# Performance work log

Hardware: AMD Instinct MI355X
Metric: run time of the kernel (lower is better)

## Reference

```python
import jax, jax.numpy as jnp
import numpy as np

V = 20000
D = 128
N_PAIRS = 65536
LOG_EPS = 1e-8


def setup_inputs() -> dict:
    key = jax.random.key(0)
    k_emb, k_i, k_j = jax.random.split(key, 3)
    # original: tf.random.uniform([V, D], 0.1, -0.1) -> uniform in (-0.1, 0.1)
    embedding = jax.random.uniform(k_emb, (V, D), dtype=jnp.float32) * 0.2 - 0.1
    i_vec = jax.random.randint(k_i, (N_PAIRS,), 0, V, dtype=jnp.int64)
    j_vec = jax.random.randint(k_j, (N_PAIRS,), 0, V, dtype=jnp.int64)
    return {"embedding": embedding, "i_vec": i_vec, "j_vec": j_vec}


def reference(embedding, i_vec, j_vec):
    # norms[i] = exp( sum_j e_i . e_j )  -- full V x V Gram matrix row-reduced
    gram = jnp.matmul(embedding, embedding.T)        # [V, V]
    norms = jnp.exp(jnp.sum(gram, axis=1))           # [V]
    # denoms[p] = exp( e_{i_p} . e_{j_p} )
    denoms = jnp.exp(jnp.sum(embedding[i_vec] * embedding[j_vec], axis=1))  # [N]
    emb_cost = -jnp.log(denoms / norms[i_vec] + LOG_EPS)
    return jnp.mean(emb_cost)
```

## Files before the change

### kernel.cpp

```cpp
#include <hip/hip_runtime.h>
#include <math.h>

#define DIM     128
#define V_ROWS  20000
#define NPAIRS  65536
#define NFLOAT4 (V_ROWS * DIM / 4)

constexpr int K1_BLOCKS  = 128;
constexpr int K1_THREADS = 512;
constexpr int K1_STRIDE  = K1_BLOCKS * K1_THREADS;
constexpr int K1_TAIL    = NFLOAT4 - 9 * K1_STRIDE;

constexpr int K2_BLOCKS  = 512;
constexpr int K2_THREADS = 512;


__global__ __launch_bounds__(K1_THREADS) void k1_colsum(
        const float4* __restrict__ emb4,
        float* __restrict__ partial) {
    const int tid = blockIdx.x * K1_THREADS + threadIdx.x;
    float4 a0 = make_float4(0.f, 0.f, 0.f, 0.f);
    float4 a1 = a0;
    #pragma unroll
    for (int k = 0; k < 8; k += 2) {
        const float4 v0 = emb4[tid + (k + 0) * K1_STRIDE];
        const float4 v1 = emb4[tid + (k + 1) * K1_STRIDE];
        a0.x += v0.x; a0.y += v0.y; a0.z += v0.z; a0.w += v0.w;
        a1.x += v1.x; a1.y += v1.y; a1.z += v1.z; a1.w += v1.w;
    }
    {
        const float4 v0 = emb4[tid + 8 * K1_STRIDE];
        a0.x += v0.x; a0.y += v0.y; a0.z += v0.z; a0.w += v0.w;
        if (tid < K1_TAIL) {
            const float4 v1 = emb4[tid + 9 * K1_STRIDE];
            a1.x += v1.x; a1.y += v1.y; a1.z += v1.z; a1.w += v1.w;
        }
    }
    float4 a = make_float4(a0.x + a1.x, a0.y + a1.y,
                           a0.z + a1.z, a0.w + a1.w);
    a.x += __shfl_xor(a.x, 32);
    a.y += __shfl_xor(a.y, 32);
    a.z += __shfl_xor(a.z, 32);
    a.w += __shfl_xor(a.w, 32);

    __shared__ float sm[8][DIM];
    const int wid  = threadIdx.x >> 6;
    const int lane = threadIdx.x & 63;
    const int col  = (threadIdx.x * 4) & 127;
    if (lane < 32) {
        sm[wid][col + 0] = a.x;
        sm[wid][col + 1] = a.y;
        sm[wid][col + 2] = a.z;
        sm[wid][col + 3] = a.w;
    }
    __syncthreads();
    if (threadIdx.x < DIM) {
        float tot = 0.f;
        #pragma unroll
        for (int w = 0; w < 8; ++w) tot += sm[w][threadIdx.x];
        partial[blockIdx.x * DIM + threadIdx.x] = tot;
    }
}

__global__ __launch_bounds__(K2_THREADS) void k2_pairs(
        const float4* __restrict__ emb4,
        const int* __restrict__ iv,
        const int* __restrict__ jv,
        const float4* __restrict__ partial4,
        float* __restrict__ blockpart) {
    const int lane = threadIdx.x & 63;
    const int wid  = threadIdx.x >> 6;

    __shared__ float4 sm4[16][32];
    __shared__ float  S_lds[DIM];
    __shared__ float  ls[8];

    {
        const int f4c = threadIdx.x & 31;
        const int g   = threadIdx.x >> 5;
        float4 c0 = make_float4(0.f, 0.f, 0.f, 0.f);
        float4 c1 = c0;
        #pragma unroll
        for (int k = 0; k < 8; k += 2) {
            const float4 v0 = partial4[(g + 16 * (k + 0)) * 32 + f4c];
            const float4 v1 = partial4[(g + 16 * (k + 1)) * 32 + f4c];
            c0.x += v0.x; c0.y += v0.y; c0.z += v0.z; c0.w += v0.w;
            c1.x += v1.x; c1.y += v1.y; c1.z += v1.z; c1.w += v1.w;
        }
        float4 s;
        s.x = c0.x + c1.x; s.y = c0.y + c1.y;
        s.z = c0.z + c1.z; s.w = c0.w + c1.w;
        sm4[g][f4c] = s;
        __syncthreads();
        if (threadIdx.x < DIM) {
            const float* smf = reinterpret_cast<const float*>(sm4);
            float tot = 0.f;
            #pragma unroll
            for (int g2 = 0; g2 < 16; ++g2) tot += smf[g2 * DIM + threadIdx.x];
            S_lds[threadIdx.x] = tot;
        }
        __syncthreads();
    }

    const int c    = lane & 15;
    const int grp  = lane >> 4;
    const int gw   = blockIdx.x * 8 + wid;
    const int base = gw * 16;

    const float4* S4 = reinterpret_cast<const float4*>(S_lds);
    const float4 s0 = S4[c * 2], s1 = S4[c * 2 + 1];

    int idxval = 0;
    if (lane < 16)      idxval = iv[base + lane];
    else if (lane < 32) idxval = jv[base + lane - 16];

    float4 A0[4], A1[4], B0[4], B1[4];
    #pragma unroll
    for (int it = 0; it < 4; ++it) {
        const int q = it * 4 + grp;
        const int i = __shfl(idxval, q);
        const int j = __shfl(idxval, 16 + q);
        const float4* ei = emb4 + (size_t)i * 32;
        const float4* ej = emb4 + (size_t)j * 32;
        A0[it] = ei[c * 2]; A1[it] = ei[c * 2 + 1];
        B0[it] = ej[c * 2]; B1[it] = ej[c * 2 + 1];
    }

    float acc = 0.f;
    #pragma unroll
    for (int it = 0; it < 4; ++it) {
        float d = A0[it].x * B0[it].x + A0[it].y * B0[it].y
                + A0[it].z * B0[it].z + A0[it].w * B0[it].w
                + A1[it].x * B1[it].x + A1[it].y * B1[it].y
                + A1[it].z * B1[it].z + A1[it].w * B1[it].w;
        float n = A0[it].x * s0.x + A0[it].y * s0.y
                + A0[it].z * s0.z + A0[it].w * s0.w
                + A1[it].x * s1.x + A1[it].y * s1.y
                + A1[it].z * s1.z + A1[it].w * s1.w;
        #pragma unroll
        for (int off = 8; off > 0; off >>= 1) {
            d += __shfl_xor(d, off);
            n += __shfl_xor(n, off);
        }
        const float cost = -__logf(__expf(d - n) + 1e-8f);
        if (c == 0) acc += cost;
    }
    acc += __shfl_xor(acc, 16);
    acc += __shfl_xor(acc, 32);

    if (lane == 0) ls[wid] = acc;
    __syncthreads();
    if (threadIdx.x == 0) {
        float s = 0.f;
        #pragma unroll
        for (int w = 0; w < 8; ++w) s += ls[w];
        blockpart[blockIdx.x] = s;
    }
}

__global__ __launch_bounds__(256) void k3_final(
        const float* __restrict__ blockpart,
        float* __restrict__ out) {
    const int t = threadIdx.x;
    float s = blockpart[t] + blockpart[t + 256];
    #pragma unroll
    for (int off = 32; off > 0; off >>= 1) s += __shfl_xor(s, off);
    __shared__ float ls[4];
    if ((t & 63) == 0) ls[t >> 6] = s;
    __syncthreads();
    if (t == 0)
        out[0] = (ls[0] + ls[1] + ls[2] + ls[3]) / (float)NPAIRS;
}

extern "C" void kernel_launch(void* const* d_in, const int* in_sizes, int n_in,
                              void* d_out, int out_size, void* d_ws, size_t ws_size,
                              hipStream_t stream) {
    const float4* emb4 = (const float4*)d_in[0];
    const int*    iv   = (const int*)d_in[1];
    const int*    jv   = (const int*)d_in[2];
    float* out = (float*)d_out;

    float* partial   = (float*)d_ws;
    float* blockpart = partial + K1_BLOCKS * DIM;

    hipLaunchKernelGGL(k1_colsum, dim3(K1_BLOCKS), dim3(K1_THREADS), 0, stream,
                       emb4, partial);
    hipLaunchKernelGGL(k2_pairs, dim3(K2_BLOCKS), dim3(K2_THREADS), 0, stream,
                       emb4, iv, jv, (const float4*)partial, blockpart);
    hipLaunchKernelGGL(k3_final, dim3(1), dim3(256), 0, stream,
                       blockpart, out);
}
```

Measured before the change: 20.66 us.

## Fold final reduction into pair kernel via packed fixed-point atomic counter

```diff
diff --git a/kernel.cpp b/kernel.cpp
--- a/kernel.cpp
+++ b/kernel.cpp
@@ -14,10 +14,15 @@
 constexpr int K2_BLOCKS  = 512;
 constexpr int K2_THREADS = 512;
 
+#define FXS 1048576.0
+
 
 __global__ __launch_bounds__(K1_THREADS) void k1_colsum(
         const float4* __restrict__ emb4,
-        float* __restrict__ partial) {
+        float* __restrict__ partial,
+        unsigned long long* __restrict__ accPack) {
+    if (blockIdx.x == 0 && threadIdx.x == 0) *accPack = 0ull;
+
     const int tid = blockIdx.x * K1_THREADS + threadIdx.x;
     float4 a0 = make_float4(0.f, 0.f, 0.f, 0.f);
     float4 a1 = a0;
@@ -67,7 +72,8 @@
         const int* __restrict__ iv,
         const int* __restrict__ jv,
         const float4* __restrict__ partial4,
-        float* __restrict__ blockpart) {
+        unsigned long long* __restrict__ accPack,
+        float* __restrict__ out) {
     const int lane = threadIdx.x & 63;
     const int wid  = threadIdx.x >> 6;
 
@@ -151,25 +157,18 @@
     if (lane == 0) ls[wid] = acc;
     __syncthreads();
     if (threadIdx.x == 0) {
-        float s = 0.f;
-        #pragma unroll
-        for (int w = 0; w < 8; ++w) s += ls[w];
-        blockpart[blockIdx.x] = s;
+        const double bsum = (double)(((ls[0] + ls[1]) + (ls[2] + ls[3])) +
+                                     ((ls[4] + ls[5]) + (ls[6] + ls[7])));
+        const long long q = __double2ll_rn(bsum * FXS);
+        const unsigned long long addend =
+            ((unsigned long long)(long long)q << 10) + 1ull;
+        const unsigned long long old = atomicAdd(accPack, addend);
+        if ((old & 1023ull) == (unsigned long long)(K2_BLOCKS - 1)) {
+            const unsigned long long tot = old + addend;
+            const long long sq = ((long long)tot) >> 10;
+            out[0] = (float)((double)sq * (1.0 / FXS) / (double)NPAIRS);
+        }
     }
-}
-
-__global__ __launch_bounds__(256) void k3_final(
-        const float* __restrict__ blockpart,
-        float* __restrict__ out) {
-    const int t = threadIdx.x;
-    float s = blockpart[t] + blockpart[t + 256];
-    #pragma unroll
-    for (int off = 32; off > 0; off >>= 1) s += __shfl_xor(s, off);
-    __shared__ float ls[4];
-    if ((t & 63) == 0) ls[t >> 6] = s;
-    __syncthreads();
-    if (t == 0)
-        out[0] = (ls[0] + ls[1] + ls[2] + ls[3]) / (float)NPAIRS;
 }
 
 extern "C" void kernel_launch(void* const* d_in, const int* in_sizes, int n_in,
@@ -180,13 +179,11 @@
     const int*    jv   = (const int*)d_in[2];
     float* out = (float*)d_out;
 
-    float* partial   = (float*)d_ws;
-    float* blockpart = partial + K1_BLOCKS * DIM;
+    unsigned long long* accPack = (unsigned long long*)d_ws;
+    float* partial = (float*)((char*)d_ws + 32);
 
     hipLaunchKernelGGL(k1_colsum, dim3(K1_BLOCKS), dim3(K1_THREADS), 0, stream,
-                       emb4, partial);
+                       emb4, partial, accPack);
     hipLaunchKernelGGL(k2_pairs, dim3(K2_BLOCKS), dim3(K2_THREADS), 0, stream,
-                       emb4, iv, jv, (const float4*)partial, blockpart);
-    hipLaunchKernelGGL(k3_final, dim3(1), dim3(256), 0, stream,
-                       blockpart, out);
+                       emb4, iv, jv, (const float4*)partial, accPack, out);
 }
```

New measurement: 22.60 us. +9.4%, slower.
